# Optimization experiments

Measured on AMD Instinct MI355X. Metric: run time of the kernel, lower is better.

Reference implementation:

```python
import jax, jax.numpy as jnp
import numpy as np

B, N, E = 32, 2048, 768
OUT = 384
SPARSITY = 4
LOCAL_C = (E + SPARSITY - 1) // SPARSITY  # 192
HID = 16
LN_EPS = 1e-5


def _layernorm(x, w, b):
    mu = jnp.mean(x, axis=-1, keepdims=True)
    var = jnp.mean(jnp.square(x - mu), axis=-1, keepdims=True)
    return (x - mu) * jax.lax.rsqrt(var + LN_EPS) * w + b


def setup_inputs() -> dict:
    key = jax.random.key(0)
    ks = jax.random.split(key, 8)
    s = 0.02
    return {
        "x": jax.random.normal(ks[0], (B, N, E), dtype=jnp.float32),
        # global head: Linear(E,16) -> LN(16) -> GELU -> Linear(16,1)
        "w_g1": jax.random.normal(ks[1], (E, HID), dtype=jnp.float32) * s,
        "b_g1": jnp.zeros((HID,), dtype=jnp.float32),
        "ln_g_w": jnp.ones((HID,), dtype=jnp.float32),
        "ln_g_b": jnp.zeros((HID,), dtype=jnp.float32),
        "w_g2": jax.random.normal(ks[2], (HID, 1), dtype=jnp.float32) * s,
        "b_g2": jnp.zeros((1,), dtype=jnp.float32),
        # local head: Linear(192,384) -> LN(384) -> GELU
        "w_l": jax.random.normal(ks[3], (LOCAL_C, OUT), dtype=jnp.float32) * s,
        "b_l": jnp.zeros((OUT,), dtype=jnp.float32),
        "ln_l_w": jnp.ones((OUT,), dtype=jnp.float32),
        "ln_l_b": jnp.zeros((OUT,), dtype=jnp.float32),
    }


def reference(x, w_g1, b_g1, ln_g_w, ln_g_b, w_g2, b_g2, w_l, b_l, ln_l_w, ln_l_b):
    # local branch: strided gather -> Linear -> LN -> GELU  [B,N,OUT]
    local = x[..., ::SPARSITY]                                   # [B,N,192]
    local_feat = jax.nn.gelu(_layernorm(local @ w_l + b_l, ln_l_w, ln_l_b),
                             approximate=False)
    # global branch: Linear -> LN -> GELU -> Linear -> [B,N,1] (broadcasts)
    g = jax.nn.gelu(_layernorm(x @ w_g1 + b_g1, ln_g_w, ln_g_b),
                    approximate=False)
    global_feat = g @ w_g2 + b_g2                                # [B,N,1]
    # AdaptiveAvgPool1d(OUT) on last dim; E % OUT == 0 -> exact pairwise mean
    pooled = jnp.mean(x.reshape(B, N, OUT, E // OUT), axis=-1)   # [B,N,OUT]
    return global_feat + pooled + local_feat
```

## Files before the change

### kernel.cpp

```cpp
#include <hip/hip_runtime.h>
#include <hip/hip_bf16.h>

#define B_   32
#define N_   2048
#define E_   768
#define OUT_ 384
#define HID_ 16
constexpr int ROWS   = B_ * N_;
constexpr int TILE_M = 16;
constexpr int NT     = OUT_ / 16;
constexpr int KT_L   = 6;
constexpr int KT_G   = 24;

typedef __attribute__((ext_vector_type(8))) short bf16x8;
typedef __attribute__((ext_vector_type(4))) float f32x4;

__device__ __forceinline__ short f2bf(float f) {
  __hip_bfloat16 h = __float2bfloat16(f);
  return __builtin_bit_cast(short, h);
}

__device__ __forceinline__ float fast_erf(float x) {
  const float ax = __builtin_fabsf(x);
  const float t  = __builtin_amdgcn_rcpf(__builtin_fmaf(0.3275911f, ax, 1.0f));
  float p = __builtin_fmaf(1.061405429f, t, -1.453152027f);
  p = __builtin_fmaf(p, t, 1.421413741f);
  p = __builtin_fmaf(p, t, -0.284496736f);
  p = __builtin_fmaf(p, t, 0.254829592f);
  const float e = __expf(-ax * ax);
  const float y = __builtin_fmaf(-p * t, e, 1.0f);
  return __builtin_copysignf(y, x);
}
__device__ __forceinline__ float gelu(float v) {
  return 0.5f * v * (1.0f + fast_erf(v * 0.70710678118654752f));
}

__global__ void prep_kernel(const float* __restrict__ w_l, const float* __restrict__ w_g1,
                            short* __restrict__ wsL, short* __restrict__ wsG) {
  int t = blockIdx.x * blockDim.x + threadIdx.x;
  int wave = t >> 6, ln = t & 63;
  int kg = ln >> 4, c16 = ln & 15;
  if (wave < NT * KT_L) {
    int n = wave / KT_L, ks = wave % KT_L;
    bf16x8 v;
#pragma unroll
    for (int j = 0; j < 8; ++j) {
      int k = ks * 32 + kg * 8 + j;
      v[j] = f2bf(w_l[k * OUT_ + n * 16 + c16]);
    }
    *reinterpret_cast<bf16x8*>(&wsL[(size_t)(wave * 64 + ln) * 8]) = v;
  } else if (wave < NT * KT_L + KT_G) {
    int ks = wave - NT * KT_L;
    bf16x8 v;
#pragma unroll
    for (int j = 0; j < 8; ++j) {
      int k = ks * 32 + kg * 8 + j;
      v[j] = f2bf(w_g1[k * HID_ + c16]);
    }
    *reinterpret_cast<bf16x8*>(&wsG[(size_t)(ks * 64 + ln) * 8]) = v;
  }
}

template <bool USE_WS>
__global__ __launch_bounds__(256, 3)
void spectre_kernel(const float* __restrict__ x,
                    const float* __restrict__ w_g1, const float* __restrict__ b_g1,
                    const float* __restrict__ ln_g_w, const float* __restrict__ ln_g_b,
                    const float* __restrict__ w_g2, const float* __restrict__ b_g2,
                    const float* __restrict__ w_l, const float* __restrict__ b_l,
                    const float* __restrict__ ln_l_w, const float* __restrict__ ln_l_b,
                    const short* __restrict__ wsL, const short* __restrict__ wsG,
                    float* __restrict__ out) {
  __shared__ float xs[TILE_M * E_];
  __shared__ float red2[4][16][17];
  __shared__ float reds[4][16][2];

  const int tid = threadIdx.x;
  const int wv  = tid >> 6;
  const int ln  = tid & 63;
  const int kg  = ln >> 4;
  const int l15 = ln & 15;
  const int row0 = blockIdx.x * TILE_M;

  const float* xb = x + (size_t)row0 * E_;

#pragma unroll
  for (int r = 0; r < 4; ++r) {
    const int row = wv * 4 + r;
    const int swz = (row & 7) << 4;
#pragma unroll
    for (int t = 0; t < 3; ++t) {
      const char* g = (const char*)xb + row * 3072 + ((t * 1024 + ln * 16) ^ swz);
      __builtin_amdgcn_global_load_lds(
          (const __attribute__((address_space(1))) void*)g,
          (__attribute__((address_space(3))) void*)((char*)xs + row * 3072 + t * 1024),
          16, 0, 0);
    }
  }

  bf16x8 gbv[6];
  if constexpr (USE_WS) {
#pragma unroll
    for (int i = 0; i < 6; ++i)
      gbv[i] = *reinterpret_cast<const bf16x8*>(&wsG[((wv * 6 + i) * 64 + ln) * 8]);
  } else {
#pragma unroll
    for (int i = 0; i < 6; ++i) {
      const int ks = wv * 6 + i;
#pragma unroll
      for (int j = 0; j < 8; ++j) gbv[i][j] = f2bf(w_g1[(ks * 32 + kg * 8 + j) * HID_ + l15]);
    }
  }
  const float bg  = b_g1[l15];
  const float lgw = ln_g_w[l15];
  const float lgb = ln_g_b[l15];
  const float wg2 = w_g2[l15];
  const float bg2 = b_g2[0];
  float blv[6], lwv[6], lbv[6];
#pragma unroll
  for (int j = 0; j < 6; ++j) {
    const int col = (wv * 6 + j) * 16 + l15;
    blv[j] = b_l[col];
    lwv[j] = ln_l_w[col];
    lbv[j] = ln_l_b[col];
  }

  asm volatile("s_waitcnt vmcnt(0)" ::: "memory");
  __syncthreads();

  const char* xc = (const char*)xs;
  const int rb   = l15 * 3072;
  const int swzl = (l15 & 7) << 4;

  f32x4 accg = {0.f, 0.f, 0.f, 0.f};
#pragma unroll
  for (int i = 0; i < 6; ++i) {
    const int ks = wv * 6 + i;
    const int b0 = ks * 128 + kg * 32;
    const float4 u0 = *reinterpret_cast<const float4*>(xc + rb + (b0 ^ swzl));
    const float4 u1 = *reinterpret_cast<const float4*>(xc + rb + ((b0 + 16) ^ swzl));
    const bf16x8 a = { f2bf(u0.x), f2bf(u0.y), f2bf(u0.z), f2bf(u0.w),
                       f2bf(u1.x), f2bf(u1.y), f2bf(u1.z), f2bf(u1.w) };
    accg = __builtin_amdgcn_mfma_f32_16x16x32_bf16(a, gbv[i], accg, 0, 0, 0);
  }
#pragma unroll
  for (int r = 0; r < 4; ++r) red2[wv][kg * 4 + r][l15] = accg[r];

  bf16x8 aL[KT_L];
#pragma unroll
  for (int ks = 0; ks < KT_L; ++ks) {
#pragma unroll
    for (int j = 0; j < 8; ++j) {
      const float v = *reinterpret_cast<const float*>(
          xc + rb + ((ks * 512 + kg * 128 + j * 16) ^ swzl));
      aL[ks][j] = f2bf(v);
    }
  }

  bf16x8 bc[6], bn[6];
#pragma unroll
  for (int j = 0; j < 6; ++j) {
    if constexpr (USE_WS) {
      bc[j] = *reinterpret_cast<const bf16x8*>(&wsL[(((wv * 6 + j) * KT_L + 0) * 64 + ln) * 8]);
    } else {
#pragma unroll
      for (int jj = 0; jj < 8; ++jj)
        bc[j][jj] = f2bf(w_l[(kg * 8 + jj) * OUT_ + (wv * 6 + j) * 16 + l15]);
    }
  }

  __syncthreads();

  float gf[4];
#pragma unroll
  for (int r = 0; r < 4; ++r) {
    const int row = kg * 4 + r;
    const float y = red2[0][row][l15] + red2[1][row][l15] +
                    red2[2][row][l15] + red2[3][row][l15] + bg;
    float s = y, q = y * y;
#pragma unroll
    for (int m = 1; m < 16; m <<= 1) {
      s += __shfl_xor(s, m);
      q += __shfl_xor(q, m);
    }
    const float mean = s * (1.f / 16.f);
    const float var  = q * (1.f / 16.f) - mean * mean;
    const float rstd = rsqrtf(var + 1e-5f);
    const float vn = (y - mean) * rstd * lgw + lgb;
    float ps = gelu(vn) * wg2;
#pragma unroll
    for (int m = 1; m < 16; m <<= 1) ps += __shfl_xor(ps, m);
    gf[r] = ps + bg2;
  }

  f32x4 acc[6];
#pragma unroll
  for (int j = 0; j < 6; ++j) acc[j] = (f32x4){0.f, 0.f, 0.f, 0.f};
#pragma unroll
  for (int ks = 0; ks < KT_L; ++ks) {
    if (ks + 1 < KT_L) {
#pragma unroll
      for (int j = 0; j < 6; ++j) {
        if constexpr (USE_WS) {
          bn[j] = *reinterpret_cast<const bf16x8*>(
              &wsL[(((wv * 6 + j) * KT_L + ks + 1) * 64 + ln) * 8]);
        } else {
#pragma unroll
          for (int jj = 0; jj < 8; ++jj)
            bn[j][jj] = f2bf(w_l[((ks + 1) * 32 + kg * 8 + jj) * OUT_ + (wv * 6 + j) * 16 + l15]);
        }
      }
    }
#pragma unroll
    for (int j = 0; j < 6; ++j)
      acc[j] = __builtin_amdgcn_mfma_f32_16x16x32_bf16(aL[ks], bc[j], acc[j], 0, 0, 0);
#pragma unroll
    for (int j = 0; j < 6; ++j) bc[j] = bn[j];
  }

  float s1[4] = {0.f, 0.f, 0.f, 0.f}, s2[4] = {0.f, 0.f, 0.f, 0.f};
#pragma unroll
  for (int j = 0; j < 6; ++j) {
#pragma unroll
    for (int r = 0; r < 4; ++r) {
      const float v = acc[j][r] + blv[j];
      acc[j][r] = v;
      s1[r] += v;
      s2[r] += v * v;
    }
  }
#pragma unroll
  for (int m = 1; m < 16; m <<= 1) {
#pragma unroll
    for (int r = 0; r < 4; ++r) {
      s1[r] += __shfl_xor(s1[r], m);
      s2[r] += __shfl_xor(s2[r], m);
    }
  }
  if (l15 == 0) {
#pragma unroll
    for (int r = 0; r < 4; ++r) {
      reds[wv][kg * 4 + r][0] = s1[r];
      reds[wv][kg * 4 + r][1] = s2[r];
    }
  }
  __syncthreads();

  float meanr[4], rstdr[4];
#pragma unroll
  for (int r = 0; r < 4; ++r) {
    const int row = kg * 4 + r;
    const float t1 = reds[0][row][0] + reds[1][row][0] + reds[2][row][0] + reds[3][row][0];
    const float t2 = reds[0][row][1] + reds[1][row][1] + reds[2][row][1] + reds[3][row][1];
    meanr[r] = t1 * (1.f / 384.f);
    const float var = t2 * (1.f / 384.f) - meanr[r] * meanr[r];
    rstdr[r] = rsqrtf(var + 1e-5f);
  }
#pragma unroll
  for (int j = 0; j < 6; ++j) {
    const int col = (wv * 6 + j) * 16 + l15;
#pragma unroll
    for (int r = 0; r < 4; ++r) {
      const int row = kg * 4 + r;
      const float2 px = *reinterpret_cast<const float2*>(
          (const char*)xs + row * 3072 + ((col * 8) ^ ((row & 7) << 4)));
      const float pooled = 0.5f * (px.x + px.y);
      const float vn = (acc[j][r] - meanr[r]) * rstdr[r] * lwv[j] + lbv[j];
      out[(size_t)(row0 + row) * OUT_ + col] = gelu(vn) + gf[r] + pooled;
    }
  }
}

extern "C" void kernel_launch(void* const* d_in, const int* in_sizes, int n_in,
                              void* d_out, int out_size, void* d_ws, size_t ws_size,
                              hipStream_t stream) {
  (void)in_sizes; (void)n_in; (void)out_size;
  const float* x      = (const float*)d_in[0];
  const float* w_g1   = (const float*)d_in[1];
  const float* b_g1   = (const float*)d_in[2];
  const float* ln_g_w = (const float*)d_in[3];
  const float* ln_g_b = (const float*)d_in[4];
  const float* w_g2   = (const float*)d_in[5];
  const float* b_g2   = (const float*)d_in[6];
  const float* w_l    = (const float*)d_in[7];
  const float* b_l    = (const float*)d_in[8];
  const float* ln_l_w = (const float*)d_in[9];
  const float* ln_l_b = (const float*)d_in[10];
  float* out = (float*)d_out;

  const size_t needL = (size_t)NT * KT_L * 64 * 8;
  const size_t needG = (size_t)KT_G * 64 * 8;
  const bool use_ws = ws_size >= (needL + needG) * sizeof(short);

  short* wsL = (short*)d_ws;
  short* wsG = wsL + needL;

  const int grid = ROWS / TILE_M;
  if (use_ws) {
    prep_kernel<<<(NT * KT_L + KT_G) * 64 / 256, 256, 0, stream>>>(w_l, w_g1, wsL, wsG);
    spectre_kernel<true><<<grid, 256, 0, stream>>>(x, w_g1, b_g1, ln_g_w, ln_g_b, w_g2, b_g2,
                                                   w_l, b_l, ln_l_w, ln_l_b, wsL, wsG, out);
  } else {
    spectre_kernel<false><<<grid, 256, 0, stream>>>(x, w_g1, b_g1, ln_g_w, ln_g_b, w_g2, b_g2,
                                                    w_l, b_l, ln_l_w, ln_l_b, nullptr, nullptr, out);
  }
}
```

Baseline: 104.5 us.

## Make blocks loop over eight row tiles, prefetching the next x tile during compute

Each block now handles eight 16-row tiles in sequence and issues the asynchronous global-to-LDS load of the next x tile right after the global-head pass, so the load overlaps the local GEMM, LayerNorm and stores. The strided local slice and the pair-pooled values are packed into separate bf16 LDS buffers during the first pass. This frees the x buffer early and drops the swizzle in favour of row padding. Local-head weight fragments are double-buffered with explicit vmcnt waits, and occupancy is lowered from 3 to 2 blocks per SIMD to fit the extra LDS. Storing the pooled values in bf16 adds rounding error compared with the previous fp32 pooling.

```diff
diff --git a/kernel.cpp b/kernel.cpp
--- a/kernel.cpp
+++ b/kernel.cpp
@@ -8,9 +8,13 @@
 #define HID_ 16
 constexpr int ROWS   = B_ * N_;
 constexpr int TILE_M = 16;
+constexpr int TPB    = 8;
 constexpr int NT     = OUT_ / 16;
 constexpr int KT_L   = 6;
 constexpr int KT_G   = 24;
+constexpr int S_AL   = 200;
+constexpr int S_PL   = 392;
+constexpr int XS_W   = 772;
 
 typedef __attribute__((ext_vector_type(8))) short bf16x8;
 typedef __attribute__((ext_vector_type(4))) float f32x4;
@@ -19,6 +23,16 @@
   __hip_bfloat16 h = __float2bfloat16(f);
   return __builtin_bit_cast(short, h);
 }
+__device__ __forceinline__ float bf2f(short s) {
+  union { unsigned u; float f; } v; v.u = ((unsigned)(unsigned short)s) << 16;
+  return v.f;
+}
+
+__device__ __forceinline__ void gload_frag(bf16x8& d, const short* a) {
+  asm volatile("global_load_dwordx4 %0, %1, off" : "=&v"(d) : "v"(a));
+}
+#define WAITV(n) do { asm volatile("s_waitcnt vmcnt(" #n ")" ::: "memory"); \
+                      __builtin_amdgcn_sched_barrier(0); } while (0)
 
 __device__ __forceinline__ float fast_erf(float x) {
   const float ax = __builtin_fabsf(x);
@@ -62,7 +76,7 @@
 }
 
 template <bool USE_WS>
-__global__ __launch_bounds__(256, 3)
+__global__ __launch_bounds__(256, 2)
 void spectre_kernel(const float* __restrict__ x,
                     const float* __restrict__ w_g1, const float* __restrict__ b_g1,
                     const float* __restrict__ ln_g_w, const float* __restrict__ ln_g_b,
@@ -71,7 +85,9 @@
                     const float* __restrict__ ln_l_w, const float* __restrict__ ln_l_b,
                     const short* __restrict__ wsL, const short* __restrict__ wsG,
                     float* __restrict__ out) {
-  __shared__ float xs[TILE_M * E_];
+  __shared__ float xs[TILE_M][XS_W];
+  __shared__ short al[TILE_M * S_AL];
+  __shared__ short pl[TILE_M * S_PL];
   __shared__ float red2[4][16][17];
   __shared__ float reds[4][16][2];
 
@@ -80,36 +96,12 @@
   const int ln  = tid & 63;
   const int kg  = ln >> 4;
   const int l15 = ln & 15;
-  const int row0 = blockIdx.x * TILE_M;
-
-  const float* xb = x + (size_t)row0 * E_;
-
-#pragma unroll
-  for (int r = 0; r < 4; ++r) {
-    const int row = wv * 4 + r;
-    const int swz = (row & 7) << 4;
-#pragma unroll
-    for (int t = 0; t < 3; ++t) {
-      const char* g = (const char*)xb + row * 3072 + ((t * 1024 + ln * 16) ^ swz);
-      __builtin_amdgcn_global_load_lds(
-          (const __attribute__((address_space(1))) void*)g,
-          (__attribute__((address_space(3))) void*)((char*)xs + row * 3072 + t * 1024),
-          16, 0, 0);
-    }
-  }
 
   bf16x8 gbv[6];
   if constexpr (USE_WS) {
 #pragma unroll
     for (int i = 0; i < 6; ++i)
       gbv[i] = *reinterpret_cast<const bf16x8*>(&wsG[((wv * 6 + i) * 64 + ln) * 8]);
-  } else {
-#pragma unroll
-    for (int i = 0; i < 6; ++i) {
-      const int ks = wv * 6 + i;
-#pragma unroll
-      for (int j = 0; j < 8; ++j) gbv[i][j] = f2bf(w_g1[(ks * 32 + kg * 8 + j) * HID_ + l15]);
-    }
   }
   const float bg  = b_g1[l15];
   const float lgw = ln_g_w[l15];
@@ -124,150 +116,204 @@
     lwv[j] = ln_l_w[col];
     lbv[j] = ln_l_b[col];
   }
-
+  const short* wlp = USE_WS ? (wsL + ((size_t)(wv * 6) * KT_L * 64 + ln) * 8) : nullptr;
+
+  auto stage = [&](int t) {
+    const float* src = x + (size_t)(blockIdx.x * TPB + t) * TILE_M * E_;
+#pragma unroll
+    for (int rr = 0; rr < 4; ++rr) {
+      const int row = wv * 4 + rr;
+#pragma unroll
+      for (int c = 0; c < 3; ++c) {
+        __builtin_amdgcn_global_load_lds(
+            (const __attribute__((address_space(1))) void*)(src + row * E_ + c * 256 + ln * 4),
+            (__attribute__((address_space(3))) void*)(&xs[row][c * 256]),
+            16, 0, 0);
+      }
+    }
+  };
+
+  stage(0);
   asm volatile("s_waitcnt vmcnt(0)" ::: "memory");
   __syncthreads();
 
-  const char* xc = (const char*)xs;
-  const int rb   = l15 * 3072;
-  const int swzl = (l15 & 7) << 4;
-
-  f32x4 accg = {0.f, 0.f, 0.f, 0.f};
-#pragma unroll
-  for (int i = 0; i < 6; ++i) {
-    const int ks = wv * 6 + i;
-    const int b0 = ks * 128 + kg * 32;
-    const float4 u0 = *reinterpret_cast<const float4*>(xc + rb + (b0 ^ swzl));
-    const float4 u1 = *reinterpret_cast<const float4*>(xc + rb + ((b0 + 16) ^ swzl));
-    const bf16x8 a = { f2bf(u0.x), f2bf(u0.y), f2bf(u0.z), f2bf(u0.w),
-                       f2bf(u1.x), f2bf(u1.y), f2bf(u1.z), f2bf(u1.w) };
-    accg = __builtin_amdgcn_mfma_f32_16x16x32_bf16(a, gbv[i], accg, 0, 0, 0);
-  }
-#pragma unroll
-  for (int r = 0; r < 4; ++r) red2[wv][kg * 4 + r][l15] = accg[r];
-
-  bf16x8 aL[KT_L];
-#pragma unroll
-  for (int ks = 0; ks < KT_L; ++ks) {
-#pragma unroll
-    for (int j = 0; j < 8; ++j) {
-      const float v = *reinterpret_cast<const float*>(
-          xc + rb + ((ks * 512 + kg * 128 + j * 16) ^ swzl));
-      aL[ks][j] = f2bf(v);
-    }
-  }
-
-  bf16x8 bc[6], bn[6];
-#pragma unroll
-  for (int j = 0; j < 6; ++j) {
+  for (int t = 0; t < TPB; ++t) {
+    const size_t rowg0 = (size_t)(blockIdx.x * TPB + t) * TILE_M;
+
+    f32x4 accg = {0.f, 0.f, 0.f, 0.f};
+#pragma unroll
+    for (int i = 0; i < 6; ++i) {
+      const int ks = wv * 6 + i;
+      const float4 u0 = *reinterpret_cast<const float4*>(&xs[l15][ks * 32 + kg * 8]);
+      const float4 u1 = *reinterpret_cast<const float4*>(&xs[l15][ks * 32 + kg * 8 + 4]);
+      short2 lv;
+      lv.x = f2bf(u0.x);
+      lv.y = f2bf(u1.x);
+      *reinterpret_cast<short2*>(&al[l15 * S_AL + 8 * ks + 2 * kg]) = lv;
+      short4 pv;
+      pv.x = f2bf(0.5f * (u0.x + u0.y));
+      pv.y = f2bf(0.5f * (u0.z + u0.w));
+      pv.z = f2bf(0.5f * (u1.x + u1.y));
+      pv.w = f2bf(0.5f * (u1.z + u1.w));
+      *reinterpret_cast<short4*>(&pl[l15 * S_PL + ks * 16 + kg * 4]) = pv;
+      const bf16x8 a = { lv.x, f2bf(u0.y), f2bf(u0.z), f2bf(u0.w),
+                         lv.y, f2bf(u1.y), f2bf(u1.z), f2bf(u1.w) };
+      bf16x8 b;
+      if constexpr (USE_WS) {
+        b = gbv[i];
+      } else {
+#pragma unroll
+        for (int j = 0; j < 8; ++j) b[j] = f2bf(w_g1[(ks * 32 + kg * 8 + j) * HID_ + l15]);
+      }
+      accg = __builtin_amdgcn_mfma_f32_16x16x32_bf16(a, b, accg, 0, 0, 0);
+    }
+#pragma unroll
+    for (int r = 0; r < 4; ++r) red2[wv][kg * 4 + r][l15] = accg[r];
+
+    __syncthreads();
+
+    if (t + 1 < TPB) stage(t + 1);
+
+    bf16x8 aL[KT_L];
+#pragma unroll
+    for (int ks = 0; ks < KT_L; ++ks)
+      aL[ks] = *reinterpret_cast<const bf16x8*>(&al[l15 * S_AL + ks * 32 + kg * 8]);
+
+    bf16x8 fA[6], fB[6];
     if constexpr (USE_WS) {
-      bc[j] = *reinterpret_cast<const bf16x8*>(&wsL[(((wv * 6 + j) * KT_L + 0) * 64 + ln) * 8]);
-    } else {
-#pragma unroll
-      for (int jj = 0; jj < 8; ++jj)
-        bc[j][jj] = f2bf(w_l[(kg * 8 + jj) * OUT_ + (wv * 6 + j) * 16 + l15]);
-    }
-  }
-
-  __syncthreads();
-
-  float gf[4];
-#pragma unroll
-  for (int r = 0; r < 4; ++r) {
-    const int row = kg * 4 + r;
-    const float y = red2[0][row][l15] + red2[1][row][l15] +
-                    red2[2][row][l15] + red2[3][row][l15] + bg;
-    float s = y, q = y * y;
-#pragma unroll
-    for (int m = 1; m < 16; m <<= 1) {
-      s += __shfl_xor(s, m);
-      q += __shfl_xor(q, m);
-    }
-    const float mean = s * (1.f / 16.f);
-    const float var  = q * (1.f / 16.f) - mean * mean;
-    const float rstd = rsqrtf(var + 1e-5f);
-    const float vn = (y - mean) * rstd * lgw + lgb;
-    float ps = gelu(vn) * wg2;
-#pragma unroll
-    for (int m = 1; m < 16; m <<= 1) ps += __shfl_xor(ps, m);
-    gf[r] = ps + bg2;
-  }
-
-  f32x4 acc[6];
-#pragma unroll
-  for (int j = 0; j < 6; ++j) acc[j] = (f32x4){0.f, 0.f, 0.f, 0.f};
-#pragma unroll
-  for (int ks = 0; ks < KT_L; ++ks) {
-    if (ks + 1 < KT_L) {
-#pragma unroll
-      for (int j = 0; j < 6; ++j) {
-        if constexpr (USE_WS) {
-          bn[j] = *reinterpret_cast<const bf16x8*>(
-              &wsL[(((wv * 6 + j) * KT_L + ks + 1) * 64 + ln) * 8]);
-        } else {
-#pragma unroll
-          for (int jj = 0; jj < 8; ++jj)
-            bn[j][jj] = f2bf(w_l[((ks + 1) * 32 + kg * 8 + jj) * OUT_ + (wv * 6 + j) * 16 + l15]);
-        }
-      }
-    }
-#pragma unroll
-    for (int j = 0; j < 6; ++j)
-      acc[j] = __builtin_amdgcn_mfma_f32_16x16x32_bf16(aL[ks], bc[j], acc[j], 0, 0, 0);
-#pragma unroll
-    for (int j = 0; j < 6; ++j) bc[j] = bn[j];
-  }
-
-  float s1[4] = {0.f, 0.f, 0.f, 0.f}, s2[4] = {0.f, 0.f, 0.f, 0.f};
-#pragma unroll
-  for (int j = 0; j < 6; ++j) {
-#pragma unroll
-    for (int r = 0; r < 4; ++r) {
-      const float v = acc[j][r] + blv[j];
-      acc[j][r] = v;
-      s1[r] += v;
-      s2[r] += v * v;
-    }
-  }
-#pragma unroll
-  for (int m = 1; m < 16; m <<= 1) {
-#pragma unroll
-    for (int r = 0; r < 4; ++r) {
-      s1[r] += __shfl_xor(s1[r], m);
-      s2[r] += __shfl_xor(s2[r], m);
-    }
-  }
-  if (l15 == 0) {
-#pragma unroll
-    for (int r = 0; r < 4; ++r) {
-      reds[wv][kg * 4 + r][0] = s1[r];
-      reds[wv][kg * 4 + r][1] = s2[r];
-    }
-  }
-  __syncthreads();
-
-  float meanr[4], rstdr[4];
-#pragma unroll
-  for (int r = 0; r < 4; ++r) {
-    const int row = kg * 4 + r;
-    const float t1 = reds[0][row][0] + reds[1][row][0] + reds[2][row][0] + reds[3][row][0];
-    const float t2 = reds[0][row][1] + reds[1][row][1] + reds[2][row][1] + reds[3][row][1];
-    meanr[r] = t1 * (1.f / 384.f);
-    const float var = t2 * (1.f / 384.f) - meanr[r] * meanr[r];
-    rstdr[r] = rsqrtf(var + 1e-5f);
-  }
-#pragma unroll
-  for (int j = 0; j < 6; ++j) {
-    const int col = (wv * 6 + j) * 16 + l15;
+#pragma unroll
+      for (int j = 0; j < 6; ++j) gload_frag(fA[j], wlp + (j * 6 + 0) * 512);
+#pragma unroll
+      for (int j = 0; j < 6; ++j) gload_frag(fB[j], wlp + (j * 6 + 1) * 512);
+    }
+
+    float gf[4];
 #pragma unroll
     for (int r = 0; r < 4; ++r) {
       const int row = kg * 4 + r;
-      const float2 px = *reinterpret_cast<const float2*>(
-          (const char*)xs + row * 3072 + ((col * 8) ^ ((row & 7) << 4)));
-      const float pooled = 0.5f * (px.x + px.y);
-      const float vn = (acc[j][r] - meanr[r]) * rstdr[r] * lwv[j] + lbv[j];
-      out[(size_t)(row0 + row) * OUT_ + col] = gelu(vn) + gf[r] + pooled;
-    }
+      const float y = red2[0][row][l15] + red2[1][row][l15] +
+                      red2[2][row][l15] + red2[3][row][l15] + bg;
+      float s = y, q = y * y;
+#pragma unroll
+      for (int m = 1; m < 16; m <<= 1) {
+        s += __shfl_xor(s, m);
+        q += __shfl_xor(q, m);
+      }
+      const float mean = s * (1.f / 16.f);
+      const float var  = q * (1.f / 16.f) - mean * mean;
+      const float rstd = rsqrtf(var + 1e-5f);
+      const float vn = (y - mean) * rstd * lgw + lgb;
+      float ps = gelu(vn) * wg2;
+#pragma unroll
+      for (int m = 1; m < 16; m <<= 1) ps += __shfl_xor(ps, m);
+      gf[r] = ps + bg2;
+    }
+
+    f32x4 acc[6];
+#pragma unroll
+    for (int j = 0; j < 6; ++j) acc[j] = (f32x4){0.f, 0.f, 0.f, 0.f};
+
+    if constexpr (USE_WS) {
+      WAITV(6);
+#pragma unroll
+      for (int j = 0; j < 6; ++j)
+        acc[j] = __builtin_amdgcn_mfma_f32_16x16x32_bf16(aL[0], fA[j], acc[j], 0, 0, 0);
+#pragma unroll
+      for (int j = 0; j < 6; ++j) gload_frag(fA[j], wlp + (j * 6 + 2) * 512);
+      WAITV(6);
+#pragma unroll
+      for (int j = 0; j < 6; ++j)
+        acc[j] = __builtin_amdgcn_mfma_f32_16x16x32_bf16(aL[1], fB[j], acc[j], 0, 0, 0);
+#pragma unroll
+      for (int j = 0; j < 6; ++j) gload_frag(fB[j], wlp + (j * 6 + 3) * 512);
+      WAITV(6);
+#pragma unroll
+      for (int j = 0; j < 6; ++j)
+        acc[j] = __builtin_amdgcn_mfma_f32_16x16x32_bf16(aL[2], fA[j], acc[j], 0, 0, 0);
+#pragma unroll
+      for (int j = 0; j < 6; ++j) gload_frag(fA[j], wlp + (j * 6 + 4) * 512);
+      WAITV(6);
+#pragma unroll
+      for (int j = 0; j < 6; ++j)
+        acc[j] = __builtin_amdgcn_mfma_f32_16x16x32_bf16(aL[3], fB[j], acc[j], 0, 0, 0);
+#pragma unroll
+      for (int j = 0; j < 6; ++j) gload_frag(fB[j], wlp + (j * 6 + 5) * 512);
+      WAITV(6);
+#pragma unroll
+      for (int j = 0; j < 6; ++j)
+        acc[j] = __builtin_amdgcn_mfma_f32_16x16x32_bf16(aL[4], fA[j], acc[j], 0, 0, 0);
+      WAITV(0);
+#pragma unroll
+      for (int j = 0; j < 6; ++j)
+        acc[j] = __builtin_amdgcn_mfma_f32_16x16x32_bf16(aL[5], fB[j], acc[j], 0, 0, 0);
+      __builtin_amdgcn_sched_barrier(0);
+    } else {
+#pragma unroll
+      for (int ks = 0; ks < KT_L; ++ks) {
+#pragma unroll
+        for (int j = 0; j < 6; ++j) {
+          const int ng = wv * 6 + j;
+          bf16x8 b;
+#pragma unroll
+          for (int jj = 0; jj < 8; ++jj)
+            b[jj] = f2bf(w_l[(ks * 32 + kg * 8 + jj) * OUT_ + ng * 16 + l15]);
+          acc[j] = __builtin_amdgcn_mfma_f32_16x16x32_bf16(aL[ks], b, acc[j], 0, 0, 0);
+        }
+      }
+      asm volatile("s_waitcnt vmcnt(0)" ::: "memory");
+      __builtin_amdgcn_sched_barrier(0);
+    }
+
+    float s1[4] = {0.f, 0.f, 0.f, 0.f}, s2[4] = {0.f, 0.f, 0.f, 0.f};
+#pragma unroll
+    for (int j = 0; j < 6; ++j) {
+#pragma unroll
+      for (int r = 0; r < 4; ++r) {
+        const float v = acc[j][r] + blv[j];
+        acc[j][r] = v;
+        s1[r] += v;
+        s2[r] += v * v;
+      }
+    }
+#pragma unroll
+    for (int m = 1; m < 16; m <<= 1) {
+#pragma unroll
+      for (int r = 0; r < 4; ++r) {
+        s1[r] += __shfl_xor(s1[r], m);
+        s2[r] += __shfl_xor(s2[r], m);
+      }
+    }
+    if (l15 == 0) {
+#pragma unroll
+      for (int r = 0; r < 4; ++r) {
+        reds[wv][kg * 4 + r][0] = s1[r];
+        reds[wv][kg * 4 + r][1] = s2[r];
+      }
+    }
+    __syncthreads();
+
+    float meanr[4], rstdr[4];
+#pragma unroll
+    for (int r = 0; r < 4; ++r) {
+      const int row = kg * 4 + r;
+      const float t1 = reds[0][row][0] + reds[1][row][0] + reds[2][row][0] + reds[3][row][0];
+      const float t2 = reds[0][row][1] + reds[1][row][1] + reds[2][row][1] + reds[3][row][1];
+      meanr[r] = t1 * (1.f / 384.f);
+      const float var = t2 * (1.f / 384.f) - meanr[r] * meanr[r];
+      rstdr[r] = rsqrtf(var + 1e-5f);
+    }
+#pragma unroll
+    for (int j = 0; j < 6; ++j) {
+      const int col = (wv * 6 + j) * 16 + l15;
+#pragma unroll
+      for (int r = 0; r < 4; ++r) {
+        const int row = kg * 4 + r;
+        const float pooled = bf2f(pl[row * S_PL + col]);
+        const float vn = (acc[j][r] - meanr[r]) * rstdr[r] * lwv[j] + lbv[j];
+        out[(rowg0 + row) * OUT_ + col] = gelu(vn) + gf[r] + pooled;
+      }
+    }
+    __syncthreads();
   }
 }
 
@@ -295,7 +341,7 @@
   short* wsL = (short*)d_ws;
   short* wsG = wsL + needL;
 
-  const int grid = ROWS / TILE_M;
+  const int grid = ROWS / (TILE_M * TPB);
   if (use_ws) {
     prep_kernel<<<(NT * KT_L + KT_G) * 64 / 256, 256, 0, stream>>>(w_l, w_g1, wsL, wsG);
     spectre_kernel<true><<<grid, 256, 0, stream>>>(x, w_g1, b_g1, ln_g_w, ln_g_b, w_g2, b_g2,
```

Measured after the change: 110.8 us. 6.1% more time.
